# Optimization experiments

Hardware: AMD Instinct MI355X
Metric: run time of the kernel (lower is better)

Reference implementation:

```python
import jax, jax.numpy as jnp
import numpy as np

B, T = 192, 50
VOCAB = 24000
EMBED = 300
HID2 = 2000          # 2*HIDDEN_SIZE
MAXOUT = 300         # DIMEN_MAXOUT_UNIT
QV = 300             # DIMEN_QUALITY_VECTOR
H2 = 100             # LSTM hidden


def setup_inputs():
    key = jax.random.key(0)
    ks = jax.random.split(key, 24)
    s = 0.02
    inp = {
        'dec_out': jax.random.normal(ks[0], (B, T, HID2), jnp.float32),
        'y': jax.random.randint(ks[1], (B, T), 0, VOCAB, jnp.int64 if jax.config.jax_enable_x64 else jnp.int32),
        'contex': jax.random.normal(ks[2], (B, T, HID2), jnp.float32),
        'embed_table': jax.random.normal(ks[3], (VOCAB, EMBED), jnp.float32) * s,
        'W1': jax.random.uniform(ks[4], (VOCAB, QV), jnp.float32),  # torch.rand
        'S_w': jax.random.normal(ks[5], (2 * MAXOUT, HID2), jnp.float32) * s,
        'S_b': jnp.zeros((2 * MAXOUT,), jnp.float32),
        'V_w': jax.random.normal(ks[6], (2 * MAXOUT, 2 * EMBED), jnp.float32) * s,
        'V_b': jnp.zeros((2 * MAXOUT,), jnp.float32),
        'C0_w': jax.random.normal(ks[7], (2 * MAXOUT, HID2), jnp.float32) * s,
        'C0_b': jnp.zeros((2 * MAXOUT,), jnp.float32),
        'W2_w': jax.random.normal(ks[8], (QV, MAXOUT), jnp.float32) * s,
        'W2_b': jnp.zeros((QV,), jnp.float32),
        'wih0': jax.random.normal(ks[9], (4 * H2, QV), jnp.float32) * s,
        'whh0': jax.random.normal(ks[10], (4 * H2, H2), jnp.float32) * s,
        'bih0': jnp.zeros((4 * H2,), jnp.float32),
        'bhh0': jnp.zeros((4 * H2,), jnp.float32),
        'wih1': jax.random.normal(ks[11], (4 * H2, H2), jnp.float32) * s,
        'whh1': jax.random.normal(ks[12], (4 * H2, H2), jnp.float32) * s,
        'bih1': jnp.zeros((4 * H2,), jnp.float32),
        'bhh1': jnp.zeros((4 * H2,), jnp.float32),
        'Wqe_w': jax.random.normal(ks[13], (1, H2), jnp.float32) * s,
        'Wqe_b': jnp.zeros((1,), jnp.float32),
    }
    return inp


def _lstm_layer(x, Wih, Whh, bih, bhh):
    # x: [B, T, D] -> outputs [B, T, H]; torch gate order i, f, g, o
    Bb = x.shape[0]
    H = Whh.shape[1]
    xT = jnp.swapaxes(x, 0, 1)  # [T, B, D]

    def step(carry, xt):
        h, c = carry
        g = xt @ Wih.T + h @ Whh.T + bih + bhh
        i, f, gg, o = jnp.split(g, 4, axis=-1)
        i = jax.nn.sigmoid(i); f = jax.nn.sigmoid(f)
        gg = jnp.tanh(gg); o = jax.nn.sigmoid(o)
        c = f * c + i * gg
        h = o * jnp.tanh(c)
        return (h, c), h

    h0 = jnp.zeros((Bb, H), x.dtype)
    (_, _), hs = jax.lax.scan(step, (h0, h0), xT)
    return jnp.swapaxes(hs, 0, 1)


def reference(dec_out, y, contex, embed_table, W1, S_w, S_b, V_w, V_b,
              C0_w, C0_b, W2_w, W2_b, wih0, whh0, bih0, bhh0,
              wih1, whh1, bih1, bhh1, Wqe_w, Wqe_b):
    Bb, Tt, _ = dec_out.shape
    embed = embed_table[y]  # [B, T, EMBED]
    idx = jnp.arange(Tt)
    li = jnp.where(idx == 0, 1, idx - 1)          # left neighbor (i==0 -> 1)
    ri = jnp.where(idx == Tt - 1, Tt - 2, idx + 1)  # right neighbor (i==T-1 -> T-2)
    tensor2 = jnp.concatenate([embed[:, li], embed[:, ri]], axis=-1)  # [B,T,600]
    t_long = (dec_out @ S_w.T + S_b) + (tensor2 @ V_w.T + V_b) + (contex @ C0_w.T + C0_b)
    # maxout over consecutive pairs: t[...,i] = max(t_long[...,2i], t_long[...,2i+1])
    t = t_long.reshape(Bb, Tt, MAXOUT, 2).max(axis=-1)
    a = t @ W2_w.T + W2_b                        # [B,T,QV]
    logits = a @ W1.T                            # [B,T,VOCAB]
    b = jax.nn.log_softmax(logits.reshape(Bb * Tt, -1), axis=1)
    quality = W1[y] * a                          # [B,T,QV]
    mask = (y == 0)
    index1 = jnp.where(mask.any(axis=1), mask.argmax(axis=1), Tt - 1)
    h = _lstm_layer(quality, wih0, whh0, bih0, bhh0)
    h = _lstm_layer(h, wih1, whh1, bih1, bhh1)   # [B,T,H2]
    s_sel = h[jnp.arange(Bb), index1]            # [B,H2]
    QE_score = jax.nn.sigmoid(s_sel @ Wqe_w.T + Wqe_b)  # [B,1]
    return (b, QE_score)
```

## Files before the change

### kernel.cpp

```cpp
#include <hip/hip_runtime.h>

typedef unsigned short u16;
typedef __attribute__((ext_vector_type(4))) float f32x4;
typedef __attribute__((ext_vector_type(8))) short bf16x8;
typedef __attribute__((ext_vector_type(4))) unsigned short u16x4;
typedef __attribute__((ext_vector_type(8))) unsigned short u16x8;

#define BT 9600
#define VOCAB 24000
#define NCB 188

__device__ __forceinline__ u16 f2b(float f){
  union { float f; unsigned u; } c; c.f = f;
  unsigned u = c.u;
  return (u16)((u + 0x7FFFu + ((u >> 16) & 1u)) >> 16);
}
__device__ __forceinline__ float b2f(u16 v){
  union { unsigned u; float f; } c; c.u = ((unsigned)v) << 16;
  return c.f;
}

#define GLD16(g, l) __builtin_amdgcn_global_load_lds( \
    (__attribute__((address_space(1))) void*)(g), \
    (__attribute__((address_space(3))) void*)(l), 16, 0, 0)

__device__ __forceinline__ void gemm_core(
    const u16* __restrict__ A, const u16* __restrict__ B,
    int K, int brow, int bcol, u16* As, u16* Bs, f32x4 acc[4][4])
{
  const int tid  = threadIdx.x & 255;
  const int w    = tid >> 6;
  const int lane = tid & 63;
  const int wm = w >> 1, wn = w & 1;

  const f32x4 fz = {0.f, 0.f, 0.f, 0.f};
  #pragma unroll
  for (int m = 0; m < 4; ++m)
    #pragma unroll
    for (int n = 0; n < 4; ++n) acc[m][n] = fz;

  const int nkt = K >> 6;

  auto stage = [&](int kt, int buf) {
    #pragma unroll
    for (int i = 0; i < 4; ++i) {
      int gl  = i * 256 + tid;
      int row = gl >> 3;
      int g   = (gl & 7) ^ (row & 7);
      const u16* ga = A + (size_t)(brow + row) * K + (kt << 6) + (g << 3);
      GLD16(ga, As + buf * 8192 + gl * 8);
      const u16* gb = B + (size_t)(bcol + row) * K + (kt << 6) + (g << 3);
      GLD16(gb, Bs + buf * 8192 + gl * 8);
    }
  };

  stage(0, 0);
  int cur = 0;
  for (int kt = 0; kt < nkt; ++kt) {
    if (kt + 1 < nkt) {
      stage(kt + 1, cur ^ 1);
      asm volatile("s_waitcnt vmcnt(8)" ::: "memory");
    } else {
      asm volatile("s_waitcnt vmcnt(0)" ::: "memory");
    }
    __builtin_amdgcn_s_barrier();
    asm volatile("" ::: "memory");
    const u16* Ab = As + cur * 8192;
    const u16* Bb = Bs + cur * 8192;
    #pragma unroll
    for (int kk = 0; kk < 2; ++kk) {
      bf16x8 af[4], bf[4];
      #pragma unroll
      for (int m = 0; m < 4; ++m) {
        int row = wm * 64 + m * 16 + (lane & 15);
        int g   = (kk * 4 + (lane >> 4)) ^ (row & 7);
        af[m] = *(const bf16x8*)(Ab + row * 64 + g * 8);
      }
      #pragma unroll
      for (int n = 0; n < 4; ++n) {
        int row = wn * 64 + n * 16 + (lane & 15);
        int g   = (kk * 4 + (lane >> 4)) ^ (row & 7);
        bf[n] = *(const bf16x8*)(Bb + row * 64 + g * 8);
      }
      #pragma unroll
      for (int m = 0; m < 4; ++m)
        #pragma unroll
        for (int n = 0; n < 4; ++n)
          acc[m][n] = __builtin_amdgcn_mfma_f32_16x16x32_bf16(af[m], bf[n], acc[m][n], 0, 0, 0);
    }
    asm volatile("" ::: "memory");
    __builtin_amdgcn_s_barrier();
    cur ^= 1;
  }
}

__device__ __forceinline__ void proj_epilogue(
    f32x4 acc[4][4], int brow, int bcol,
    const float* __restrict__ b1, const float* __restrict__ b2,
    float* __restrict__ out)
{
  int tid = threadIdx.x & 255;
  int lane = tid & 63, w = tid >> 6;
  int wm = w >> 1, wn = w & 1;
  #pragma unroll
  for (int m = 0; m < 4; ++m)
    #pragma unroll
    for (int n = 0; n < 4; ++n)
      #pragma unroll
      for (int r = 0; r < 4; ++r) {
        int row = brow + wm * 64 + m * 16 + ((lane >> 4) << 2) + r;
        int col = bcol + wn * 64 + n * 16 + (lane & 15);
        if (col < 400)
          out[(size_t)row * 400 + col] = acc[m][n][r] + b1[col] + b2[col];
      }
}

__device__ __forceinline__ void prep_main_body(
    const float* __restrict__ dec, const float* __restrict__ ctx,
    u16* __restrict__ Xcat, int tid)
{
  if (tid >= 9600 * 500) return;
  int r = tid / 500, k8 = (tid % 500) * 8;
  const float* src = (k8 < 2000) ? dec + (size_t)r * 2000 + k8
                                 : ctx + (size_t)r * 2000 + (k8 - 2000);
  const float4* s4 = (const float4*)src;
  float4 v0 = s4[0], v1 = s4[1];
  u16x8 o;
  o[0] = f2b(v0.x); o[1] = f2b(v0.y); o[2] = f2b(v0.z); o[3] = f2b(v0.w);
  o[4] = f2b(v1.x); o[5] = f2b(v1.y); o[6] = f2b(v1.z); o[7] = f2b(v1.w);
  *(u16x8*)(Xcat + (size_t)r * 4608 + k8) = o;
}

__device__ __forceinline__ void prep_emb_body(
    const int* __restrict__ y, const float* __restrict__ etab,
    u16* __restrict__ Xcat, int tid)
{
  if (tid >= 9600 * 152) return;
  int r = tid / 152, u = tid % 152;
  u16* xr = Xcat + (size_t)r * 4608;
  if (u >= 150) {
    int base = (u == 150) ? 4300 : 4604;
    u16x4 z; z[0] = 0; z[1] = 0; z[2] = 0; z[3] = 0;
    *(u16x4*)(xr + base) = z;
    return;
  }
  int t = r % 50;
  int side = u / 75, j4 = (u % 75) * 4;
  int tt = (side == 0) ? (t == 0 ? 1 : t - 1) : (t == 49 ? 48 : t + 1);
  int tok = y[r - t + tt];
  float4 v = *(const float4*)(etab + (size_t)tok * 300 + j4);
  u16x4 o; o[0] = f2b(v.x); o[1] = f2b(v.y); o[2] = f2b(v.z); o[3] = f2b(v.w);
  *(u16x4*)(xr + (side == 0 ? 4000 : 4304) + j4) = o;
}

__device__ __forceinline__ void wcat_body(
    const float* __restrict__ Sw, const float* __restrict__ C0w, const float* __restrict__ Vw,
    const float* __restrict__ Sb, const float* __restrict__ Vb, const float* __restrict__ C0b,
    u16* __restrict__ Wcat, float* __restrict__ biasc, int tid)
{
  if (tid >= 640 * 4608) return;
  int n = tid / 4608, k = tid % 4608;
  float v = 0.f;
  if (n < 600) {
    if (k < 2000)                  v = Sw[n * 2000 + k];
    else if (k < 4000)             v = C0w[n * 2000 + (k - 2000)];
    else if (k < 4300)             v = Vw[n * 600 + (k - 4000)];
    else if (k >= 4304 && k < 4604) v = Vw[n * 600 + 300 + (k - 4304)];
  }
  Wcat[tid] = f2b(v);
  if (k == 0) biasc[n] = (n < 600) ? (Sb[n] + Vb[n] + C0b[n]) : 0.f;
}

__device__ __forceinline__ void conv_body(
    const float* __restrict__ src, u16* __restrict__ dst,
    int srows, int scols, int drows, int dcols4, int tid)
{
  if (tid >= drows * dcols4) return;
  int r = tid / dcols4, c4 = (tid % dcols4) * 4;
  u16x4 o; o[0] = 0; o[1] = 0; o[2] = 0; o[3] = 0;
  if (r < srows && c4 < scols) {
    float4 v = *(const float4*)(src + (size_t)r * scols + c4);
    o[0] = f2b(v.x); o[1] = f2b(v.y); o[2] = f2b(v.z); o[3] = f2b(v.w);
  }
  *(u16x4*)(dst + (size_t)r * (dcols4 * 4) + c4) = o;
}

__global__ __launch_bounds__(256) void k_prep_all(
    const float* __restrict__ dec, const float* __restrict__ ctx,
    const int* __restrict__ y, const float* __restrict__ etab,
    const float* __restrict__ Sw, const float* __restrict__ C0w,
    const float* __restrict__ Vw, const float* __restrict__ Sb,
    const float* __restrict__ Vb, const float* __restrict__ C0b,
    const float* __restrict__ W1, const float* __restrict__ W2w,
    const float* __restrict__ wih0, const float* __restrict__ wih1,
    u16* __restrict__ Xcat, u16* __restrict__ Wcat, float* __restrict__ biasc,
    u16* __restrict__ W1b, u16* __restrict__ W2b,
    u16* __restrict__ wih0b, u16* __restrict__ wih1b)
{
  int bid = blockIdx.x, th = threadIdx.x;
  if (bid < 18750)      prep_main_body(dec, ctx, Xcat, bid * 256 + th);
  else if (bid < 24450) prep_emb_body(y, etab, Xcat, (bid - 18750) * 256 + th);
  else if (bid < 35970) wcat_body(Sw, C0w, Vw, Sb, Vb, C0b, Wcat, biasc, (bid - 24450) * 256 + th);
  else if (bid < 43490) conv_body(W1,   W1b,   24000, 300, 24064, 80, (bid - 35970) * 256 + th);
  else if (bid < 43610) conv_body(W2w,  W2b,   300,   300, 384,   80, (bid - 43490) * 256 + th);
  else if (bid < 43770) conv_body(wih0, wih0b, 400,   300, 512,   80, (bid - 43610) * 256 + th);
  else                  conv_body(wih1, wih1b, 400,   100, 512,   32, (bid - 43770) * 256 + th);
}

__global__ __launch_bounds__(256) void k_gemm_tlong(
    const u16* __restrict__ Xcat, const u16* __restrict__ Wcat,
    const float* __restrict__ biasc, u16* __restrict__ tb)
{
  __shared__ u16 As[16384], Bs[16384];
  f32x4 acc[4][4];
  int L = blockIdx.x;
  int xcd = L & 7, s = L >> 3;
  int yy = (s / 5) * 8 + xcd;
  int xx = s % 5;
  if (yy >= 75) return;
  int brow = yy * 128, bcol = xx * 128;
  gemm_core(Xcat, Wcat, 4608, brow, bcol, As, Bs, acc);
  int lane = threadIdx.x & 63, w = threadIdx.x >> 6;
  int wm = w >> 1, wn = w & 1;
  #pragma unroll
  for (int m = 0; m < 4; ++m)
    #pragma unroll
    for (int n = 0; n < 4; ++n)
      #pragma unroll
      for (int r = 0; r < 4; ++r) {
        int row = brow + wm * 64 + m * 16 + ((lane >> 4) << 2) + r;
        int col = bcol + wn * 64 + n * 16 + (lane & 15);
        float v = acc[m][n][r] + biasc[col];
        float o = __shfl_xor(v, 1);
        float t = fmaxf(v, o);
        if ((lane & 1) == 0)
          tb[(size_t)row * 320 + (col >> 1)] = f2b(t);
      }
}

__global__ __launch_bounds__(256) void k_gemm_a(
    const u16* __restrict__ tb, const u16* __restrict__ W2b,
    const float* __restrict__ W2bias, const float* __restrict__ W1,
    const int* __restrict__ y, u16* __restrict__ ab, u16* __restrict__ qb)
{
  __shared__ u16 As[16384], Bs[16384];
  f32x4 acc[4][4];
  int brow = blockIdx.y * 128, bcol = blockIdx.x * 128;
  gemm_core(tb, W2b, 320, brow, bcol, As, Bs, acc);
  int lane = threadIdx.x & 63, w = threadIdx.x >> 6;
  int wm = w >> 1, wn = w & 1;
  #pragma unroll
  for (int m = 0; m < 4; ++m)
    #pragma unroll
    for (int n = 0; n < 4; ++n)
      #pragma unroll
      for (int r = 0; r < 4; ++r) {
        int row = brow + wm * 64 + m * 16 + ((lane >> 4) << 2) + r;
        int col = bcol + wn * 64 + n * 16 + (lane & 15);
        if (col < 320) {
          float bias = (col < 300) ? W2bias[col] : 0.f;
          float a = acc[m][n][r] + bias;
          ab[(size_t)row * 320 + col] = f2b(a);
          float q = 0.f;
          if (col < 300) {
            int yv = y[row];
            q = a * W1[(size_t)yv * 300 + col];
          }
          qb[(size_t)row * 320 + col] = f2b(q);
        }
      }
}

__global__ __launch_bounds__(256) void k_gemm_logits(
    const u16* __restrict__ ab, const u16* __restrict__ W1b,
    u16* __restrict__ lb, float* __restrict__ part)
{
  __shared__ u16 smem[32768];
  __shared__ float rowsum[128][2];
  f32x4 acc[4][4];
  int g = blockIdx.x;
  int brow = (g / NCB) * 128, bcol = (g % NCB) * 128;
  gemm_core(ab, W1b, 320, brow, bcol, smem, smem + 16384, acc);
  int lane = threadIdx.x & 63, w = threadIdx.x >> 6;
  int wm = w >> 1, wn = w & 1;
  #pragma unroll
  for (int m = 0; m < 4; ++m)
    #pragma unroll
    for (int r = 0; r < 4; ++r) {
      int lrow = wm * 64 + m * 16 + ((lane >> 4) << 2) + r;
      float es = 0.f;
      #pragma unroll
      for (int n = 0; n < 4; ++n) {
        int lcol = wn * 64 + n * 16 + (lane & 15);
        float v = acc[m][n][r];
        smem[lrow * 136 + lcol] = f2b(v);
        if (bcol + lcol < VOCAB) es += __expf(v);
      }
      es += __shfl_xor(es, 1); es += __shfl_xor(es, 2);
      es += __shfl_xor(es, 4); es += __shfl_xor(es, 8);
      if ((lane & 15) == 0) rowsum[lrow][wn] = es;
    }
  __syncthreads();
  if (threadIdx.x < 128)
    part[(size_t)(brow + threadIdx.x) * NCB + (g % NCB)] =
        rowsum[threadIdx.x][0] + rowsum[threadIdx.x][1];
  #pragma unroll
  for (int j = 0; j < 8; ++j) {
    int ch   = j * 256 + threadIdx.x;
    int rowl = ch >> 4;
    int c16  = (ch & 15) << 3;
    u16x8 v = *(const u16x8*)(smem + rowl * 136 + c16);
    *(u16x8*)(lb + (size_t)(brow + rowl) * 24064 + bcol + c16) = v;
  }
}

__global__ __launch_bounds__(256) void k_rowlog(
    const float* __restrict__ part, float* __restrict__ logl)
{
  int row = blockIdx.x * 4 + (threadIdx.x >> 6);
  int l = threadIdx.x & 63;
  const float* p = part + (size_t)row * NCB;
  float s = p[l] + p[l + 64] + (l < 60 ? p[l + 128] : 0.f);
  s += __shfl_xor(s, 1);  s += __shfl_xor(s, 2);  s += __shfl_xor(s, 4);
  s += __shfl_xor(s, 8);  s += __shfl_xor(s, 16); s += __shfl_xor(s, 32);
  if (l == 0) logl[row] = logf(s);
}

__global__ __launch_bounds__(256) void k_fixup_bf16(
    const u16* __restrict__ lb, const float* __restrict__ logl,
    float* __restrict__ out)
{
  size_t i = (size_t)blockIdx.x * blockDim.x + threadIdx.x;
  size_t stride = (size_t)gridDim.x * blockDim.x;
  const size_t total = (size_t)BT * (VOCAB / 8);
  for (; i < total; i += stride) {
    size_t row = i / (VOCAB / 8);
    int c8 = (int)(i % (VOCAB / 8)) * 8;
    float l = logl[row];
    u16x8 v = *(const u16x8*)(lb + row * 24064 + c8);
    float4 o0, o1;
    o0.x = b2f(v[0]) - l; o0.y = b2f(v[1]) - l; o0.z = b2f(v[2]) - l; o0.w = b2f(v[3]) - l;
    o1.x = b2f(v[4]) - l; o1.y = b2f(v[5]) - l; o1.z = b2f(v[6]) - l; o1.w = b2f(v[7]) - l;
    float* op = out + row * VOCAB + c8;
    *(float4*)op = o0;
    *(float4*)(op + 4) = o1;
  }
}

__global__ __launch_bounds__(256) void k_gemm_proj(
    const u16* __restrict__ Ab, const u16* __restrict__ Bb, int K,
    const float* __restrict__ b1, const float* __restrict__ b2, float* __restrict__ out)
{
  __shared__ u16 As[16384], Bs[16384];
  f32x4 acc[4][4];
  int brow = blockIdx.y * 128, bcol = blockIdx.x * 128;
  gemm_core(Ab, Bb, K, brow, bcol, As, Bs, acc);
  proj_epilogue(acc, brow, bcol, b1, b2, out);
}

__global__ __launch_bounds__(512) void k_lstm0(
    const float* __restrict__ xp0, const float* __restrict__ whh0, u16* __restrict__ h0b)
{
  int b = blockIdx.x, g = threadIdx.x;
  __shared__ float h[100];
  __shared__ float act[400];
  float wrow[100];
  if (g < 400) {
    const float4* wr = (const float4*)(whh0 + (size_t)g * 100);
    #pragma unroll
    for (int q = 0; q < 25; ++q) {
      float4 t = wr[q];
      wrow[4 * q] = t.x; wrow[4 * q + 1] = t.y; wrow[4 * q + 2] = t.z; wrow[4 * q + 3] = t.w;
    }
  }
  if (g < 100) h[g] = 0.f;
  float c = 0.f;
  __syncthreads();
  for (int t = 0; t < 50; ++t) {
    if (g < 400) {
      float s = xp0[(size_t)(b * 50 + t) * 400 + g];
      const float4* hv = (const float4*)h;
      #pragma unroll
      for (int q = 0; q < 25; ++q) {
        float4 hh = hv[q];
        s += wrow[4 * q] * hh.x + wrow[4 * q + 1] * hh.y
           + wrow[4 * q + 2] * hh.z + wrow[4 * q + 3] * hh.w;
      }
      act[g] = (g >= 200 && g < 300) ? tanhf(s) : 1.f / (1.f + __expf(-s));
    }
    __syncthreads();
    if (g < 100) {
      c = act[100 + g] * c + act[g] * act[200 + g];
      float hn = act[300 + g] * tanhf(c);
      h[g] = hn;
      h0b[(size_t)(b * 50 + t) * 128 + g] = f2b(hn);
    } else if (g < 128) {
      h0b[(size_t)(b * 50 + t) * 128 + g] = 0;
    }
    __syncthreads();
  }
}

__global__ __launch_bounds__(512) void k_lstm1(
    const float* __restrict__ xp1, const float* __restrict__ whh1,
    const int* __restrict__ y, const float* __restrict__ wqe,
    const float* __restrict__ wqeb, float* __restrict__ qout)
{
  int b = blockIdx.x, g = threadIdx.x;
  __shared__ float h[100];
  __shared__ float act[400];
  __shared__ float hsel[100];
  __shared__ int idx1;
  float wrow[100];
  if (g < 400) {
    const float4* wr = (const float4*)(whh1 + (size_t)g * 100);
    #pragma unroll
    for (int q = 0; q < 25; ++q) {
      float4 t = wr[q];
      wrow[4 * q] = t.x; wrow[4 * q + 1] = t.y; wrow[4 * q + 2] = t.z; wrow[4 * q + 3] = t.w;
    }
  }
  if (g == 0) {
    int ix = 49;
    for (int t = 0; t < 50; ++t) { if (y[b * 50 + t] == 0) { ix = t; break; } }
    idx1 = ix;
  }
  if (g < 100) { h[g] = 0.f; hsel[g] = 0.f; }
  float c = 0.f;
  __syncthreads();
  for (int t = 0; t < 50; ++t) {
    if (g < 400) {
      float s = xp1[(size_t)(b * 50 + t) * 400 + g];
      const float4* hv = (const float4*)h;
      #pragma unroll
      for (int q = 0; q < 25; ++q) {
        float4 hh = hv[q];
        s += wrow[4 * q] * hh.x + wrow[4 * q + 1] * hh.y
           + wrow[4 * q + 2] * hh.z + wrow[4 * q + 3] * hh.w;
      }
      act[g] = (g >= 200 && g < 300) ? tanhf(s) : 1.f / (1.f + __expf(-s));
    }
    __syncthreads();
    if (g < 100) {
      c = act[100 + g] * c + act[g] * act[200 + g];
      float hn = act[300 + g] * tanhf(c);
      h[g] = hn;
      if (t == idx1) hsel[g] = hn;
    }
    __syncthreads();
  }
  if (g == 0) {
    float s = wqeb[0];
    for (int j = 0; j < 100; ++j) s += hsel[j] * wqe[j];
    qout[b] = 1.f / (1.f + __expf(-s));
  }
}

__global__ __launch_bounds__(256) void k_gemm_logits_f32(
    const u16* __restrict__ ab, const u16* __restrict__ W1b,
    float* __restrict__ dout, float* __restrict__ part)
{
  __shared__ u16 As[16384], Bs[16384];
  __shared__ float rowsum[128][2];
  f32x4 acc[4][4];
  int brow = blockIdx.y * 128, bcol = blockIdx.x * 128;
  gemm_core(ab, W1b, 320, brow, bcol, As, Bs, acc);
  int lane = threadIdx.x & 63, w = threadIdx.x >> 6;
  int wm = w >> 1, wn = w & 1;
  #pragma unroll
  for (int m = 0; m < 4; ++m)
    #pragma unroll
    for (int r = 0; r < 4; ++r) {
      int lrow = wm * 64 + m * 16 + ((lane >> 4) << 2) + r;
      size_t grow = (size_t)(brow + lrow);
      float es = 0.f;
      #pragma unroll
      for (int n = 0; n < 4; ++n) {
        int col = bcol + wn * 64 + n * 16 + (lane & 15);
        float v = acc[m][n][r];
        if (col < VOCAB) { dout[grow * VOCAB + col] = v; es += __expf(v); }
      }
      es += __shfl_xor(es, 1); es += __shfl_xor(es, 2);
      es += __shfl_xor(es, 4); es += __shfl_xor(es, 8);
      if ((lane & 15) == 0) rowsum[lrow][wn] = es;
    }
  __syncthreads();
  if (threadIdx.x < 128)
    part[(size_t)(brow + threadIdx.x) * NCB + blockIdx.x] =
        rowsum[threadIdx.x][0] + rowsum[threadIdx.x][1];
}

__global__ __launch_bounds__(256) void k_fixup_f32(
    float4* __restrict__ out4, const float* __restrict__ logl)
{
  size_t i = (size_t)blockIdx.x * blockDim.x + threadIdx.x;
  size_t stride = (size_t)gridDim.x * blockDim.x;
  const size_t total = (size_t)BT * (VOCAB / 4);
  for (; i < total; i += stride) {
    size_t row = i / (VOCAB / 4);
    float l = logl[row];
    float4 v = out4[i];
    v.x -= l; v.y -= l; v.z -= l; v.w -= l;
    out4[i] = v;
  }
}

extern "C" void kernel_launch(void* const* d_in, const int* in_sizes, int n_in,
                              void* d_out, int out_size, void* d_ws, size_t ws_size,
                              hipStream_t stream) {
  const float* dec  = (const float*)d_in[0];
  const int*   y    = (const int*)d_in[1];
  const float* ctx  = (const float*)d_in[2];
  const float* etab = (const float*)d_in[3];
  const float* W1   = (const float*)d_in[4];
  const float* Sw   = (const float*)d_in[5];
  const float* Sb   = (const float*)d_in[6];
  const float* Vw   = (const float*)d_in[7];
  const float* Vb   = (const float*)d_in[8];
  const float* C0w  = (const float*)d_in[9];
  const float* C0b  = (const float*)d_in[10];
  const float* W2w  = (const float*)d_in[11];
  const float* W2bias = (const float*)d_in[12];
  const float* wih0 = (const float*)d_in[13];
  const float* whh0 = (const float*)d_in[14];
  const float* bih0 = (const float*)d_in[15];
  const float* bhh0 = (const float*)d_in[16];
  const float* wih1 = (const float*)d_in[17];
  const float* whh1 = (const float*)d_in[18];
  const float* bih1 = (const float*)d_in[19];
  const float* bhh1 = (const float*)d_in[20];
  const float* wqe  = (const float*)d_in[21];
  const float* wqeb = (const float*)d_in[22];

  char* ws = (char*)d_ws;
  u16*   Xcat  = (u16*)(ws + 0);
  u16*   Wcat  = (u16*)(ws + 88473600);
  float* biasc = (float*)(ws + 94371840);
  u16*   tb    = (u16*)(ws + 94374400);
  u16*   W2b   = (u16*)(ws + 100518400);
  u16*   ab    = (u16*)(ws + 100764160);
  u16*   qb    = (u16*)(ws + 106908160);
  u16*   W1b   = (u16*)(ws + 113052160);
  float* part  = (float*)(ws + 128453120);
  float* logl  = (float*)(ws + 135672320);
  u16*   wih0b = (u16*)(ws + 135710720);
  float* xp0   = (float*)(ws + 136038400);
  u16*   h0b   = (u16*)(ws + 151398400);
  u16*   wih1b = (u16*)(ws + 153856000);
  float* xp1   = (float*)(ws + 153987072);
  u16*   lb    = (u16*)(ws + 169347072);
  const size_t WS_NEED_BF16 = 169347072ull + 462028800ull;
  const bool use_bf16_logits = (ws_size >= WS_NEED_BF16);

  float* bout  = (float*)d_out;
  float* qeout = bout + (size_t)BT * VOCAB;

  k_prep_all<<<43834, 256, 0, stream>>>(dec, ctx, y, etab, Sw, C0w, Vw, Sb, Vb, C0b,
                                        W1, W2w, wih0, wih1,
                                        Xcat, Wcat, biasc, W1b, W2b, wih0b, wih1b);

  k_gemm_tlong<<<400, 256, 0, stream>>>(Xcat, Wcat, biasc, tb);
  k_gemm_a<<<dim3(3, 75), 256, 0, stream>>>(tb, W2b, W2bias, W1, y, ab, qb);

  if (use_bf16_logits) {
    k_gemm_logits<<<14100, 256, 0, stream>>>(ab, W1b, lb, part);
    k_rowlog<<<2400, 256, 0, stream>>>(part, logl);
    k_fixup_bf16<<<4096, 256, 0, stream>>>(lb, logl, bout);
  } else {
    float* part_fb = (float*)(ws + 169347072);
    k_gemm_logits_f32<<<dim3(NCB, 75), 256, 0, stream>>>(ab, W1b, bout, part_fb);
    k_rowlog<<<2400, 256, 0, stream>>>(part_fb, logl);
    k_fixup_f32<<<4096, 256, 0, stream>>>((float4*)bout, logl);
  }

  k_gemm_proj<<<dim3(4, 75), 256, 0, stream>>>(qb, wih0b, 320, bih0, bhh0, xp0);
  k_lstm0<<<192, 512, 0, stream>>>(xp0, whh0, h0b);
  k_gemm_proj<<<dim3(4, 75), 256, 0, stream>>>(h0b, wih1b, 128, bih1, bhh1, xp1);
  k_lstm1<<<192, 512, 0, stream>>>(xp1, whh1, y, wqe, wqeb, qeout);
}
```

Measured before the change: 986.6 us.

## Compute two column tiles per block in logits GEMM with packed bf16 conversion

The logits GEMM kernel now has each block compute a 128x256 output region as two 128-column tiles. The K loops of both tiles are chained into one 10-step pipeline, so the ring of loads never drains between tiles, and the number of blocks is halved. The epilogue uses the hardware packed bf16 convert instruction instead of software rounding. This doubles the accumulator registers, which may lower occupancy. The A tile is also reloaded for the second tile rather than reused.

```diff
diff --git a/kernel.cpp b/kernel.cpp
--- a/kernel.cpp
+++ b/kernel.cpp
@@ -14,6 +14,11 @@
   union { float f; unsigned u; } c; c.f = f;
   unsigned u = c.u;
   return (u16)((u + 0x7FFFu + ((u >> 16) & 1u)) >> 16);
+}
+__device__ __forceinline__ unsigned f2b2(float a, float b){
+  unsigned r;
+  asm("v_cvt_pk_bf16_f32 %0, %1, %2" : "=v"(r) : "v"(a), "v"(b));
+  return r;
 }
 __device__ __forceinline__ float b2f(u16 v){
   union { unsigned u; float f; } c; c.u = ((unsigned)v) << 16;
@@ -271,46 +276,128 @@
       }
 }
 
-__global__ __launch_bounds__(256) void k_gemm_logits(
+__global__ __launch_bounds__(256) void k_gemm_logits2(
     const u16* __restrict__ ab, const u16* __restrict__ W1b,
     u16* __restrict__ lb, float* __restrict__ part)
 {
   __shared__ u16 smem[32768];
   __shared__ float rowsum[128][2];
-  f32x4 acc[4][4];
+  f32x4 acc0[4][4], acc1[4][4];
+  const int tid  = threadIdx.x;
+  const int w    = tid >> 6;
+  const int lane = tid & 63;
+  const int wm = w >> 1, wn = w & 1;
   int g = blockIdx.x;
-  int brow = (g / NCB) * 128, bcol = (g % NCB) * 128;
-  gemm_core(ab, W1b, 320, brow, bcol, smem, smem + 16384, acc);
-  int lane = threadIdx.x & 63, w = threadIdx.x >> 6;
-  int wm = w >> 1, wn = w & 1;
+  int brow  = (g / 94) * 128;
+  int bcol0 = (g % 94) * 256;
+
+  const f32x4 fz = {0.f, 0.f, 0.f, 0.f};
   #pragma unroll
   for (int m = 0; m < 4; ++m)
     #pragma unroll
-    for (int r = 0; r < 4; ++r) {
-      int lrow = wm * 64 + m * 16 + ((lane >> 4) << 2) + r;
-      float es = 0.f;
+    for (int n = 0; n < 4; ++n) { acc0[m][n] = fz; acc1[m][n] = fz; }
+
+  auto stagev = [&](int vt, int buf) {
+    int kt   = (vt >= 5) ? vt - 5 : vt;
+    int bcol = bcol0 + ((vt >= 5) ? 128 : 0);
+    #pragma unroll
+    for (int i = 0; i < 4; ++i) {
+      int gl  = i * 256 + tid;
+      int row = gl >> 3;
+      int gs  = (gl & 7) ^ (row & 7);
+      const u16* ga = ab  + (size_t)(brow + row) * 320 + (kt << 6) + (gs << 3);
+      GLD16(ga, smem + buf * 8192 + gl * 8);
+      const u16* gb = W1b + (size_t)(bcol + row) * 320 + (kt << 6) + (gs << 3);
+      GLD16(gb, smem + 16384 + buf * 8192 + gl * 8);
+    }
+  };
+
+  stagev(0, 0);
+  int cur = 0;
+  for (int vt = 0; vt < 10; ++vt) {
+    if (vt + 1 < 10) {
+      stagev(vt + 1, cur ^ 1);
+      asm volatile("s_waitcnt vmcnt(8)" ::: "memory");
+    } else {
+      asm volatile("s_waitcnt vmcnt(0)" ::: "memory");
+    }
+    __builtin_amdgcn_s_barrier();
+    asm volatile("" ::: "memory");
+    const u16* Ab = smem + cur * 8192;
+    const u16* Bb = smem + 16384 + cur * 8192;
+    f32x4 (*acc)[4] = (vt < 5) ? acc0 : acc1;
+    #pragma unroll
+    for (int kk = 0; kk < 2; ++kk) {
+      bf16x8 af[4], bf[4];
+      #pragma unroll
+      for (int m = 0; m < 4; ++m) {
+        int row = wm * 64 + m * 16 + (lane & 15);
+        int gs  = (kk * 4 + (lane >> 4)) ^ (row & 7);
+        af[m] = *(const bf16x8*)(Ab + row * 64 + gs * 8);
+      }
+      #pragma unroll
+      for (int n = 0; n < 4; ++n) {
+        int row = wn * 64 + n * 16 + (lane & 15);
+        int gs  = (kk * 4 + (lane >> 4)) ^ (row & 7);
+        bf[n] = *(const bf16x8*)(Bb + row * 64 + gs * 8);
+      }
+      #pragma unroll
+      for (int m = 0; m < 4; ++m)
+        #pragma unroll
+        for (int n = 0; n < 4; ++n)
+          acc[m][n] = __builtin_amdgcn_mfma_f32_16x16x32_bf16(af[m], bf[n], acc[m][n], 0, 0, 0);
+    }
+    asm volatile("" ::: "memory");
+    __builtin_amdgcn_s_barrier();
+    cur ^= 1;
+  }
+
+  #pragma unroll
+  for (int t = 0; t < 2; ++t) {
+    f32x4 (*acc)[4] = (t == 0) ? acc0 : acc1;
+    int bcol = bcol0 + t * 128;
+    int cb   = (g % 94) * 2 + t;
+    #pragma unroll
+    for (int m = 0; m < 4; ++m)
+      #pragma unroll
+      for (int r = 0; r < 4; ++r) {
+        int lrow = wm * 64 + m * 16 + ((lane >> 4) << 2) + r;
+        float es = 0.f;
+        #pragma unroll
+        for (int n = 0; n < 4; ++n) {
+          int lcol = wn * 64 + n * 16 + (lane & 15);
+          if (bcol + lcol < VOCAB) es += __expf(acc[m][n][r]);
+        }
+        es += __shfl_xor(es, 1); es += __shfl_xor(es, 2);
+        es += __shfl_xor(es, 4); es += __shfl_xor(es, 8);
+        if ((lane & 15) == 0) rowsum[lrow][wn] = es;
+      }
+    #pragma unroll
+    for (int m = 0; m < 4; ++m) {
+      int lrow0 = wm * 64 + m * 16 + ((lane >> 4) << 2);
       #pragma unroll
       for (int n = 0; n < 4; ++n) {
         int lcol = wn * 64 + n * 16 + (lane & 15);
-        float v = acc[m][n][r];
-        smem[lrow * 136 + lcol] = f2b(v);
-        if (bcol + lcol < VOCAB) es += __expf(v);
-      }
-      es += __shfl_xor(es, 1); es += __shfl_xor(es, 2);
-      es += __shfl_xor(es, 4); es += __shfl_xor(es, 8);
-      if ((lane & 15) == 0) rowsum[lrow][wn] = es;
-    }
-  __syncthreads();
-  if (threadIdx.x < 128)
-    part[(size_t)(brow + threadIdx.x) * NCB + (g % NCB)] =
-        rowsum[threadIdx.x][0] + rowsum[threadIdx.x][1];
-  #pragma unroll
-  for (int j = 0; j < 8; ++j) {
-    int ch   = j * 256 + threadIdx.x;
-    int rowl = ch >> 4;
-    int c16  = (ch & 15) << 3;
-    u16x8 v = *(const u16x8*)(smem + rowl * 136 + c16);
-    *(u16x8*)(lb + (size_t)(brow + rowl) * 24064 + bcol + c16) = v;
+        unsigned p01 = f2b2(acc[m][n][0], acc[m][n][1]);
+        unsigned p23 = f2b2(acc[m][n][2], acc[m][n][3]);
+        smem[(lrow0 + 0) * 136 + lcol] = (u16)p01;
+        smem[(lrow0 + 1) * 136 + lcol] = (u16)(p01 >> 16);
+        smem[(lrow0 + 2) * 136 + lcol] = (u16)p23;
+        smem[(lrow0 + 3) * 136 + lcol] = (u16)(p23 >> 16);
+      }
+    }
+    __syncthreads();
+    if (tid < 128)
+      part[(size_t)(brow + tid) * NCB + cb] = rowsum[tid][0] + rowsum[tid][1];
+    #pragma unroll
+    for (int j = 0; j < 8; ++j) {
+      int ch   = j * 256 + tid;
+      int rowl = ch >> 4;
+      int c16  = (ch & 15) << 3;
+      u16x8 v = *(const u16x8*)(smem + rowl * 136 + c16);
+      *(u16x8*)(lb + (size_t)(brow + rowl) * 24064 + bcol + c16) = v;
+    }
+    __syncthreads();
   }
 }
 
@@ -563,7 +650,7 @@
   k_gemm_a<<<dim3(3, 75), 256, 0, stream>>>(tb, W2b, W2bias, W1, y, ab, qb);
 
   if (use_bf16_logits) {
-    k_gemm_logits<<<14100, 256, 0, stream>>>(ab, W1b, lb, part);
+    k_gemm_logits2<<<7050, 256, 0, stream>>>(ab, W1b, lb, part);
     k_rowlog<<<2400, 256, 0, stream>>>(part, logl);
     k_fixup_bf16<<<4096, 256, 0, stream>>>(lb, logl, bout);
   } else {
```

Result: slower. 1.039 ms (+5.3%).
